# Optimization experiments

Measured on AMD Instinct MI355X. Metric: run time of the kernel, lower is better.

## Reference

```python
import jax, jax.numpy as jnp
import numpy as np

N_QUBIT = 14
N_LAYER = 16
BATCH = 512
DIM = 2 ** N_QUBIT

# wire 0 is the most-significant bit (deepquantum convention: state.reshape([2]*n), wire i = axis i)
_bits = (np.arange(DIM)[:, None] >> (N_QUBIT - 1 - np.arange(N_QUBIT))) & 1
SIGNS = jnp.asarray(2.0 * _bits - 1.0, dtype=jnp.float32)  # (DIM, n_qubit), -1 for bit=0, +1 for bit=1


def _apply_1q(state, gate, w):
    # state: (B, DIM) complex64; gate: (2,2) complex
    B = state.shape[0]
    left, right = 2 ** w, 2 ** (N_QUBIT - w - 1)
    st = state.reshape(B, left, 2, right)
    return jnp.einsum('ab,xlbr->xlar', gate, st).reshape(B, DIM)


def _cnot(state, c, t):
    # CNOT control c, target t: X on target where control bit = 1
    B = state.shape[0]
    st = state.reshape((B,) + (2,) * N_QUBIT)
    ax_c, ax_t = c + 1, t + 1
    a0 = jnp.take(st, 0, axis=ax_c)
    a1 = jnp.take(st, 1, axis=ax_c)
    a1 = jnp.flip(a1, axis=ax_t if ax_t < ax_c else ax_t - 1)  # flip size-2 axis == X gate
    return jnp.stack([a0, a1], axis=ax_c).reshape(B, DIM)


def _rz_layer(state, thetas):
    # RZ(th) = diag(e^{-i th/2}, e^{+i th/2}) on every wire -> single fused diagonal phase
    return state * jnp.exp(0.5j * (SIGNS @ thetas))


def _ry_layer(state, thetas):
    for w in range(N_QUBIT):
        c = jnp.cos(thetas[w] * 0.5)
        s = jnp.sin(thetas[w] * 0.5)
        gate = jnp.stack([jnp.stack([c, -s]), jnp.stack([s, c])]).astype(jnp.complex64)
        state = _apply_1q(state, gate, w)
    return state


def _circuit(z, theta):
    state = z.reshape(z.shape[0], DIM)
    for l in range(N_LAYER):
        state = _rz_layer(state, theta[l, 0])
        state = _ry_layer(state, theta[l, 1])
        state = _rz_layer(state, theta[l, 2])
        for w in range(N_QUBIT):  # cnot_ring
            state = _cnot(state, w, (w + 1) % N_QUBIT)
    return state


def _split(state, w):
    B = state.shape[0]
    st = state.reshape(B, 2 ** w, 2, 2 ** (N_QUBIT - w - 1))
    return st[:, :, 0, :], st[:, :, 1, :]


def _expectations(state):
    outs = []
    for w in (0, 1):  # <Z_w> = sum |psi_0|^2 - |psi_1|^2
        p0, p1 = _split(state, w)
        outs.append(jnp.sum(jnp.abs(p0) ** 2 - jnp.abs(p1) ** 2, axis=(1, 2)))
    cross0 = None
    for w in (0, 1):  # <X_w> = 2 Re sum conj(psi_0) psi_1
        p0, p1 = _split(state, w)
        cr = jnp.conj(p0) * p1
        if w == 0:
            cross0 = cr
        outs.append(2.0 * jnp.sum(jnp.real(cr), axis=(1, 2)))
    outs.append(2.0 * jnp.sum(jnp.imag(cross0), axis=(1, 2)))  # <Y_0> = 2 Im sum conj(psi_0) psi_1
    return jnp.stack(outs, axis=1).astype(jnp.float32)  # (B, 5)


def setup_inputs() -> dict:
    key = jax.random.key(0)
    k1, k2, k3, k4 = jax.random.split(key, 4)
    zr = jax.random.normal(k1, (BATCH, DIM), dtype=jnp.float32)
    zi = jax.random.normal(k2, (BATCH, DIM), dtype=jnp.float32)
    z = (zr + 1j * zi).astype(jnp.complex64)
    z = z / jnp.linalg.norm(z, axis=1, keepdims=True)  # normalized quantum states
    z = z[:, :, None]  # (B, 2^n, 1) per docstring
    theta = jax.random.normal(k3, (N_LAYER, 3, N_QUBIT), dtype=jnp.float32)
    y = jax.random.randint(k4, (BATCH,), 0, 5)
    return {"z": z, "theta": theta, "y": y}


def reference(z, theta, y):
    state = _circuit(z, theta)
    output = _expectations(state)
    logp = jax.nn.log_softmax(output, axis=1)
    loss = -jnp.mean(jnp.take_along_axis(logp, y[:, None], axis=1))
    return (loss, output)
```

## Files before the change

kernel.cpp:

```cpp
#include <hip/hip_runtime.h>
#include <hip/hip_bf16.h>

#define NQ     14
#define DIM    16384
#define NLAYER 16
#define BATCH  512
#define NT     1024

typedef float v2f __attribute__((ext_vector_type(2)));

__device__ __forceinline__ constexpr int POSB(int x){ return (x ^ ((x >> 5) & 31)) << 3; }

__device__ __forceinline__ float bf2f(unsigned int u16){
  union { unsigned int i; float f; } v; v.i = u16 << 16; return v.f;
}

__device__ __forceinline__ float thv(const void* th, int i, bool b16){
  return b16 ? bf2f(((const unsigned short*)th)[i]) : ((const float*)th)[i];
}

__device__ int srcF(int x){
  int v = x;
  #pragma unroll
  for (int k = 13; k >= 0; --k){
    int tb = 13 - ((k + 1) % 14);
    v ^= ((v >> (13 - k)) & 1) << tb;
  }
  return v;
}

__device__ __forceinline__ v2f cmul(v2f a, v2f b){
  v2f t, d;
  asm("v_pk_mul_f32 %0, %1, %2 op_sel:[0,0] op_sel_hi:[1,0]"
      : "=v"(t) : "v"(a), "v"(b));
  asm("v_pk_fma_f32 %0, %1, %2, %3 op_sel:[1,1,0] op_sel_hi:[0,1,1] neg_lo:[0,1,0]"
      : "=v"(d) : "v"(a), "v"(b), "v"(t));
  return d;
}

__device__ __forceinline__ void rot2(v2f& a0, v2f& a1, float c, float s){
  v2f c2 = (v2f){c, c}, s2 = (v2f){s, s};
  v2f t0 = a0;
  a0 = a0 * c2 - a1 * s2;
  a1 = t0 * s2 + a1 * c2;
}

__global__ __launch_bounds__(NT) __attribute__((amdgpu_waves_per_eu(4, 4)))
void qnn_circuit(const void* __restrict__ zraw,
                 const void* __restrict__ theta,
                 float* __restrict__ out)
{
  __shared__ v2f   S[DIM];
  __shared__ v2f   ph0H[128], ph0L[128], ph2H[128], ph2Lt[128];
  __shared__ float csT[28];
  __shared__ int   sHB[128], sLB[128];
  __shared__ float red[16*5];

  char* Sb = (char*)S;
  const int t = threadIdx.x;
  const int b = blockIdx.x;

  int pred = 0;
  if (t < 336){
    unsigned int w  = ((const unsigned int*)theta)[t];
    unsigned int lo = w & 0xffffu;
    unsigned int e  = (lo >> 7) & 0xffu;
    pred = (e >= 100 && e <= 140) || (lo == 0);
  }
  const bool th_b16 = (__syncthreads_count(pred) > 250);

  pred = 0;
  if (t < 256){
    unsigned int w  = ((const unsigned int*)zraw)[t];
    unsigned int lo = w & 0xffffu;
    unsigned int e  = (lo >> 7) & 0xffu;
    pred = (e >= 88 && e <= 140) || (lo == 0);
  }
  const bool z_b16 = (__syncthreads_count(pred) > 160);

  if (t < 128){ sHB[t] = POSB(srcF(t << 7)); sLB[t] = POSB(srcF(t)); }

  if (z_b16){
    const uint4* zb = (const uint4*)((const unsigned short*)zraw + (size_t)b * (DIM * 2));
    #pragma unroll 1
    for (int jj = 0; jj < 4; ++jj){
      int x4 = t + NT * jj;
      uint4 w = zb[x4];
      int xb = x4 * 4;
      *(v2f*)(Sb + POSB(xb+0)) = (v2f){bf2f(w.x & 0xffffu), bf2f(w.x >> 16)};
      *(v2f*)(Sb + POSB(xb+1)) = (v2f){bf2f(w.y & 0xffffu), bf2f(w.y >> 16)};
      *(v2f*)(Sb + POSB(xb+2)) = (v2f){bf2f(w.z & 0xffffu), bf2f(w.z >> 16)};
      *(v2f*)(Sb + POSB(xb+3)) = (v2f){bf2f(w.w & 0xffffu), bf2f(w.w >> 16)};
    }
  } else {
    const float4* zf = (const float4*)((const float*)zraw + (size_t)b * DIM);
    #pragma unroll 1
    for (int jj = 0; jj < 4; ++jj){
      int x4 = t + NT * jj;
      float4 w = zf[x4];
      int xb = x4 * 4;
      *(v2f*)(Sb + POSB(xb+0)) = (v2f){w.x, 0.f};
      *(v2f*)(Sb + POSB(xb+1)) = (v2f){w.y, 0.f};
      *(v2f*)(Sb + POSB(xb+2)) = (v2f){w.z, 0.f};
      *(v2f*)(Sb + POSB(xb+3)) = (v2f){w.w, 0.f};
    }
  }
  __syncthreads();

  const int pwb = POSB(t);
  const int hb  = t >> 7;
  const int slB = sLB[t & 127];

  const int pb2 = POSB(((t >> 7) << 10) | (t & 127));
  const int pb3 = POSB(((t >> 7) << 10) | (((t >> 5) & 1) << 9)
                     | (((t >> 4) & 1) << 8) | (((t >> 6) & 1) << 7) | (t & 15));
  const int pbM = POSB(t << 4);
  const int rM  = t & 7;
  const int hbM = t >> 3;

  for (int l = 0; l < NLAYER; ++l){
    const int thb = l * 42;

    if (t < 512){
      int grp = t >> 7, idx = t & 127;
      int tz = thb + ((grp >= 2) ? 28 : 0);
      float ph = 0.f;
      if ((grp & 1) == 0){
        #pragma unroll
        for (int w = 0; w < 7; ++w)
          ph += (((idx >> (6 - w)) & 1) ? 0.5f : -0.5f) * thv(theta, tz + w, th_b16);
      } else {
        #pragma unroll
        for (int w = 7; w < 14; ++w)
          ph += (((idx >> (13 - w)) & 1) ? 0.5f : -0.5f) * thv(theta, tz + w, th_b16);
      }
      float sn, cs; sincosf(ph, &sn, &cs);
      v2f v = (v2f){cs, sn};
      if      (grp == 0) ph0H[idx] = v;
      else if (grp == 1) ph0L[idx] = v;
      else if (grp == 2) ph2H[idx] = v;
      else               ph2Lt[((idx & 15) << 3) | (idx >> 4)] = v;
    } else if (t < 512 + 14){
      int q = t - 512;
      float sn, cs; sincosf(0.5f * thv(theta, thb + 14 + q, th_b16), &sn, &cs);
      csT[2*q] = cs; csT[2*q+1] = sn;
    }

    {
      v2f g[16];
      if (l == 0){
        #pragma unroll
        for (int j = 0; j < 16; ++j) g[j] = *(v2f*)(Sb + (pwb ^ (j << 13)));
      } else {
        #pragma unroll
        for (int j = 0; j < 16; ++j)
          g[j] = *(v2f*)(Sb + (sHB[hb + 8*j] ^ slB));
      }
      __syncthreads();

      {
        v2f cl = ph0L[t & 127];
        #pragma unroll
        for (int j = 0; j < 16; ++j)
          g[j] = cmul(g[j], cmul(ph0H[hb + 8*j], cl));
      }
      #pragma unroll
      for (int q = 0; q < 4; ++q){
        float c = csT[2*q], sn = csT[2*q+1];
        int m = 8 >> q;
        #pragma unroll
        for (int j = 0; j < 16; ++j){
          if (j & m) continue;
          rot2(g[j], g[j | m], c, sn);
        }
      }
      #pragma unroll
      for (int j = 0; j < 16; ++j) *(v2f*)(Sb + (pwb ^ (j << 13))) = g[j];
    }
    __syncthreads();

    #pragma unroll 1
    for (int it = 0; it < 2; ++it){
      int pb = pb2 ^ (it << 16);
      v2f h[8];
      #pragma unroll
      for (int j = 0; j < 8; ++j) h[j] = *(v2f*)(Sb + (pb ^ (((j << 7) | (j << 2)) << 3)));
      #pragma unroll
      for (int q = 0; q < 3; ++q){
        float c = csT[2*(4+q)], sn = csT[2*(4+q)+1];
        int m = 4 >> q;
        #pragma unroll
        for (int j = 0; j < 8; ++j){
          if (j & m) continue;
          rot2(h[j], h[j | m], c, sn);
        }
      }
      #pragma unroll
      for (int j = 0; j < 8; ++j) *(v2f*)(Sb + (pb ^ (((j << 7) | (j << 2)) << 3))) = h[j];
    }
    __syncthreads();

    #pragma unroll 1
    for (int it = 0; it < 2; ++it){
      int pb = pb3 ^ (it << 16);
      v2f h[8];
      #pragma unroll
      for (int j = 0; j < 8; ++j) h[j] = *(v2f*)(Sb + (pb ^ (((j << 4) | (j >> 1)) << 3)));
      #pragma unroll
      for (int q = 0; q < 3; ++q){
        float c = csT[2*(7+q)], sn = csT[2*(7+q)+1];
        int m = 4 >> q;
        #pragma unroll
        for (int j = 0; j < 8; ++j){
          if (j & m) continue;
          rot2(h[j], h[j | m], c, sn);
        }
      }
      #pragma unroll
      for (int j = 0; j < 8; ++j) *(v2f*)(Sb + (pb ^ (((j << 4) | (j >> 1)) << 3))) = h[j];
    }
    __syncthreads();

    {
      v2f h[16];
      #pragma unroll
      for (int j = 0; j < 16; ++j) h[j] = *(v2f*)(Sb + (pbM ^ (j << 3)));
      #pragma unroll
      for (int q = 0; q < 4; ++q){
        float c = csT[2*(10+q)], sn = csT[2*(10+q)+1];
        int m = 8 >> q;
        #pragma unroll
        for (int j = 0; j < 16; ++j){
          if (j & m) continue;
          rot2(h[j], h[j | m], c, sn);
        }
      }
      {
        v2f chh = ph2H[hbM];
        #pragma unroll
        for (int j = 0; j < 16; ++j)
          h[j] = cmul(h[j], cmul(chh, ph2Lt[(j << 3) | rM]));
      }
      #pragma unroll
      for (int j = 0; j < 16; ++j) *(v2f*)(Sb + (pbM ^ (j << 3))) = h[j];
    }
    __syncthreads();
  }

  float z0=0.f, z1=0.f, x0s=0.f, x1s=0.f, y0s=0.f;
  {
    v2f g[16];
    #pragma unroll
    for (int j = 0; j < 16; ++j)
      g[j] = *(v2f*)(Sb + (sHB[hb + 8*j] ^ slB));

    #pragma unroll
    for (int j = 0; j < 16; ++j){
      float pw = g[j].x*g[j].x + g[j].y*g[j].y;
      z0 += (j & 8) ? -pw : pw;
      z1 += (j & 4) ? -pw : pw;
    }
    #pragma unroll
    for (int j = 0; j < 8; ++j){
      v2f p0 = g[j], p1 = g[j+8];
      x0s += 2.f*(p0.x*p1.x + p0.y*p1.y);
      y0s += 2.f*(p0.x*p1.y - p0.y*p1.x);
    }
    #pragma unroll
    for (int j = 0; j < 16; ++j){
      if (j & 4) continue;
      v2f p0 = g[j], p1 = g[j|4];
      x1s += 2.f*(p0.x*p1.x + p0.y*p1.y);
    }
  }
  #pragma unroll
  for (int o = 32; o >= 1; o >>= 1){
    z0  += __shfl_down(z0,  o, 64);
    z1  += __shfl_down(z1,  o, 64);
    x0s += __shfl_down(x0s, o, 64);
    x1s += __shfl_down(x1s, o, 64);
    y0s += __shfl_down(y0s, o, 64);
  }
  int wid = t >> 6, lane = t & 63;
  if (lane == 0){
    red[wid*5+0]=z0; red[wid*5+1]=z1; red[wid*5+2]=x0s; red[wid*5+3]=x1s; red[wid*5+4]=y0s;
  }
  __syncthreads();
  if (t < 5){
    float sum = 0.f;
    #pragma unroll
    for (int w = 0; w < 16; ++w) sum += red[w*5 + t];
    out[1 + b*5 + t] = sum;
  }
}

__global__ __launch_bounds__(512)
void qnn_loss(const int* __restrict__ y, float* __restrict__ out)
{
  __shared__ float red[8];
  int t = threadIdx.x;
  const float* o = out + 1 + t*5;
  float o0=o[0], o1=o[1], o2=o[2], o3=o[3], o4=o[4];
  float m = fmaxf(fmaxf(fmaxf(o0,o1), fmaxf(o2,o3)), o4);
  float sum = expf(o0-m)+expf(o1-m)+expf(o2-m)+expf(o3-m)+expf(o4-m);
  float lse = m + logf(sum);
  int yi = y[t]; yi = yi < 0 ? 0 : (yi > 4 ? 4 : yi);
  float lb = lse - o[yi];

  #pragma unroll
  for (int ofs = 32; ofs >= 1; ofs >>= 1) lb += __shfl_down(lb, ofs, 64);
  if ((t & 63) == 0) red[t >> 6] = lb;
  __syncthreads();
  if (t == 0){
    float s = 0.f;
    #pragma unroll
    for (int w = 0; w < 8; ++w) s += red[w];
    out[0] = s / (float)BATCH;
  }
}

extern "C" void kernel_launch(void* const* d_in, const int* in_sizes, int n_in,
                              void* d_out, int out_size, void* d_ws, size_t ws_size,
                              hipStream_t stream)
{
  const void* z     = d_in[0];
  const void* theta = d_in[1];
  const int*  y     = (const int*)d_in[2];
  float*      out   = (float*)d_out;

  qnn_circuit<<<BATCH, NT, 0, stream>>>(z, theta, out);
  qnn_loss<<<1, 512, 0, stream>>>(y, out);
}
```

Baseline: 267.2 us.

## Regroup middle RY stages into wave-local passes with block fences instead of barriers

The three middle RY passes (wires 4-13) are remapped so each 64-thread wavefront owns a contiguous 1024-amplitude slab. The passes become 4+4+2 qubit groups, which lets two __syncthreads barriers be replaced by __threadfence_block. The phase table layout for the final RZ is changed to match the new thread mapping. This cuts block-wide barrier cost per layer, but correctness now relies on each wave only touching its own slab and on fence semantics within a wavefront.

```diff
diff --git a/kernel.cpp b/kernel.cpp
--- a/kernel.cpp
+++ b/kernel.cpp
@@ -111,12 +111,12 @@
   const int hb  = t >> 7;
   const int slB = sLB[t & 127];
 
-  const int pb2 = POSB(((t >> 7) << 10) | (t & 127));
-  const int pb3 = POSB(((t >> 7) << 10) | (((t >> 5) & 1) << 9)
-                     | (((t >> 4) & 1) << 8) | (((t >> 6) & 1) << 7) | (t & 15));
-  const int pbM = POSB(t << 4);
-  const int rM  = t & 7;
-  const int hbM = t >> 3;
+  const int wv  = t >> 6, L = t & 63;
+  const int pbA  = POSB((wv << 10) | L);
+  const int pbB1 = POSB((wv << 10) | ((L >> 2) << 6) | (L & 3));
+  const int pbB2 = POSB((wv << 10) | (L << 2));
+  const int hB2  = (wv << 3) | (L >> 5);
+  const int rB2  = L & 31;
 
   for (int l = 0; l < NLAYER; ++l){
     const int thb = l * 42;
@@ -139,7 +139,7 @@
       if      (grp == 0) ph0H[idx] = v;
       else if (grp == 1) ph0L[idx] = v;
       else if (grp == 2) ph2H[idx] = v;
-      else               ph2Lt[((idx & 15) << 3) | (idx >> 4)] = v;
+      else               ph2Lt[((idx & 3) << 5) | (idx >> 2)] = v;
     } else if (t < 512 + 14){
       int q = t - 512;
       float sn, cs; sincosf(0.5f * thv(theta, thb + 14 + q, th_b16), &sn, &cs);
@@ -179,55 +179,13 @@
     }
     __syncthreads();
 
-    #pragma unroll 1
-    for (int it = 0; it < 2; ++it){
-      int pb = pb2 ^ (it << 16);
-      v2f h[8];
-      #pragma unroll
-      for (int j = 0; j < 8; ++j) h[j] = *(v2f*)(Sb + (pb ^ (((j << 7) | (j << 2)) << 3)));
-      #pragma unroll
-      for (int q = 0; q < 3; ++q){
-        float c = csT[2*(4+q)], sn = csT[2*(4+q)+1];
-        int m = 4 >> q;
-        #pragma unroll
-        for (int j = 0; j < 8; ++j){
-          if (j & m) continue;
-          rot2(h[j], h[j | m], c, sn);
-        }
-      }
-      #pragma unroll
-      for (int j = 0; j < 8; ++j) *(v2f*)(Sb + (pb ^ (((j << 7) | (j << 2)) << 3))) = h[j];
-    }
-    __syncthreads();
-
-    #pragma unroll 1
-    for (int it = 0; it < 2; ++it){
-      int pb = pb3 ^ (it << 16);
-      v2f h[8];
-      #pragma unroll
-      for (int j = 0; j < 8; ++j) h[j] = *(v2f*)(Sb + (pb ^ (((j << 4) | (j >> 1)) << 3)));
-      #pragma unroll
-      for (int q = 0; q < 3; ++q){
-        float c = csT[2*(7+q)], sn = csT[2*(7+q)+1];
-        int m = 4 >> q;
-        #pragma unroll
-        for (int j = 0; j < 8; ++j){
-          if (j & m) continue;
-          rot2(h[j], h[j | m], c, sn);
-        }
-      }
-      #pragma unroll
-      for (int j = 0; j < 8; ++j) *(v2f*)(Sb + (pb ^ (((j << 4) | (j >> 1)) << 3))) = h[j];
-    }
-    __syncthreads();
-
     {
       v2f h[16];
       #pragma unroll
-      for (int j = 0; j < 16; ++j) h[j] = *(v2f*)(Sb + (pbM ^ (j << 3)));
+      for (int j = 0; j < 16; ++j) h[j] = *(v2f*)(Sb + (pbA ^ ((j << 9) | (j << 4))));
       #pragma unroll
       for (int q = 0; q < 4; ++q){
-        float c = csT[2*(10+q)], sn = csT[2*(10+q)+1];
+        float c = csT[2*(4+q)], sn = csT[2*(4+q)+1];
         int m = 8 >> q;
         #pragma unroll
         for (int j = 0; j < 16; ++j){
@@ -235,14 +193,63 @@
           rot2(h[j], h[j | m], c, sn);
         }
       }
-      {
-        v2f chh = ph2H[hbM];
-        #pragma unroll
-        for (int j = 0; j < 16; ++j)
-          h[j] = cmul(h[j], cmul(chh, ph2Lt[(j << 3) | rM]));
-      }
-      #pragma unroll
-      for (int j = 0; j < 16; ++j) *(v2f*)(Sb + (pbM ^ (j << 3))) = h[j];
+      #pragma unroll
+      for (int j = 0; j < 16; ++j) *(v2f*)(Sb + (pbA ^ ((j << 9) | (j << 4)))) = h[j];
+    }
+    __threadfence_block();
+
+    {
+      v2f h[16];
+      #pragma unroll
+      for (int j = 0; j < 16; ++j)
+        h[j] = *(v2f*)(Sb + (pbB1 ^ ((j << 5) ^ ((j >> 3) << 3))));
+      #pragma unroll
+      for (int q = 0; q < 4; ++q){
+        float c = csT[2*(8+q)], sn = csT[2*(8+q)+1];
+        int m = 8 >> q;
+        #pragma unroll
+        for (int j = 0; j < 16; ++j){
+          if (j & m) continue;
+          rot2(h[j], h[j | m], c, sn);
+        }
+      }
+      #pragma unroll
+      for (int j = 0; j < 16; ++j)
+        *(v2f*)(Sb + (pbB1 ^ ((j << 5) ^ ((j >> 3) << 3)))) = h[j];
+    }
+    __threadfence_block();
+
+    {
+      v2f h[16];
+      #pragma unroll
+      for (int i = 0; i < 4; ++i){
+        int gb = pbB2 ^ ((i << 11) | (i << 6));
+        #pragma unroll
+        for (int j = 0; j < 4; ++j) h[i*4+j] = *(v2f*)(Sb + (gb ^ (j << 3)));
+      }
+      #pragma unroll
+      for (int q = 0; q < 2; ++q){
+        float c = csT[2*(12+q)], sn = csT[2*(12+q)+1];
+        int m = 2 >> q;
+        #pragma unroll
+        for (int r = 0; r < 16; ++r){
+          if ((r & 3) & m) continue;
+          rot2(h[r], h[r | m], c, sn);
+        }
+      }
+      #pragma unroll
+      for (int i = 0; i < 4; ++i){
+        v2f chh = ph2H[hB2 | (i << 1)];
+        #pragma unroll
+        for (int j = 0; j < 4; ++j)
+          h[i*4+j] = cmul(h[i*4+j], cmul(chh, ph2Lt[(j << 5) | rB2]));
+      }
+      #pragma unroll
+      for (int i = 0; i < 4; ++i){
+        int gb = pbB2 ^ ((i << 11) | (i << 6));
+        #pragma unroll
+        for (int j = 0; j < 4; ++j) *(v2f*)(Sb + (gb ^ (j << 3))) = h[i*4+j];
+      }
     }
     __syncthreads();
   }
```

Result: no change. 264.3 us (-1.1%).
